# Kernel tuning notes

Measured on AMD Instinct MI355X. Metric: run time of the kernel, lower is better.

## Reference

```python
import jax, jax.numpy as jnp
import numpy as np

ALPHA = 0.5

def setup_inputs() -> dict:
    key = jax.random.key(0)
    k1, k2, k3 = jax.random.split(key, 3)
    B, C = 16384, 4096
    logits = jax.random.normal(k1, (B, C), dtype=jnp.float32)
    targets = jax.random.randint(k2, (B,), 0, C)
    hierarchy_matrix = jax.random.uniform(k3, (C, C), dtype=jnp.float32)
    return {"logits": logits, "targets": targets, "hierarchy_matrix": hierarchy_matrix}

def reference(logits, targets, hierarchy_matrix):
    # Cross-entropy (mean reduction)
    logp = jax.nn.log_softmax(logits, axis=-1)  # [B, C]
    ce = -jnp.take_along_axis(logp, targets[:, None], axis=-1).squeeze(-1).mean()
    # Hierarchical penalty: mean_i sum_c probs[i,c] * (1 + H[targets[i], c])
    probs = jnp.exp(logp)                        # [B, C]
    hier = hierarchy_matrix[targets]             # gather rows -> [B, C]
    penalty = (probs * (1.0 + hier)).sum(axis=-1).mean()
    return (1.0 - ALPHA) * ce + ALPHA * penalty
```

## Files before the change

### kernel.cpp

```cpp
#include <hip/hip_runtime.h>


#define ALPHA       0.5f
#define NCOLS       4096
#define WPB         4
#define BLOCK_THR   (WPB * 64)

__global__ __launch_bounds__(BLOCK_THR)
void hier_loss_partial(const float* __restrict__ logits,
                       const int*   __restrict__ targets,
                       const float* __restrict__ hmat,
                       float*       __restrict__ partials,
                       float inv_b)
{
    const int row  = blockIdx.x * WPB + (threadIdx.x >> 6);
    const int lane = threadIdx.x & 63;

    const float* __restrict__ lrow = logits + (size_t)row * NCOLS;
    const int    tgt               = targets[row];
    const float* __restrict__ hrow = hmat + (size_t)tgt * NCOLS;

    const float lt = lrow[tgt];

    const float4* __restrict__ l4 = reinterpret_cast<const float4*>(lrow);
    const float4* __restrict__ h4 = reinterpret_cast<const float4*>(hrow);

    float se = 0.0f;
    float sh = 0.0f;

    #pragma unroll
    for (int c = 0; c < 4; ++c) {
        float4 lv[4], hv[4];
        #pragma unroll
        for (int j = 0; j < 4; ++j) {
            lv[j] = l4[(c * 4 + j) * 64 + lane];
            hv[j] = h4[(c * 4 + j) * 64 + lane];
        }
        #pragma unroll
        for (int j = 0; j < 4; ++j) {
            const float e0 = __expf(lv[j].x);
            const float e1 = __expf(lv[j].y);
            const float e2 = __expf(lv[j].z);
            const float e3 = __expf(lv[j].w);
            se += (e0 + e1) + (e2 + e3);
            sh += e0 * hv[j].x + e1 * hv[j].y + e2 * hv[j].z + e3 * hv[j].w;
        }
    }

    #pragma unroll
    for (int off = 1; off < 64; off <<= 1) {
        se += __shfl_xor(se, off);
        sh += __shfl_xor(sh, off);
    }

    if (lane == 0) {
        const float ce  = __logf(se) - lt;
        const float pen = 1.0f + sh / se;
        partials[row] = ((1.0f - ALPHA) * ce + ALPHA * pen) * inv_b;
    }
}

__global__ __launch_bounds__(1024)
void hier_loss_reduce(const float* __restrict__ partials,
                      float*       __restrict__ out,
                      int n4)
{
    const int tid  = threadIdx.x;
    const int wave = tid >> 6;
    const int lane = tid & 63;

    const float4* __restrict__ p4 = reinterpret_cast<const float4*>(partials);
    float s = 0.0f;
    for (int i = tid; i < n4; i += 1024) {
        const float4 v = p4[i];
        s += (v.x + v.y) + (v.z + v.w);
    }

    #pragma unroll
    for (int off = 1; off < 64; off <<= 1)
        s += __shfl_xor(s, off);

    __shared__ float ss[16];
    if (lane == 0) ss[wave] = s;
    __syncthreads();

    if (tid == 0) {
        float acc = 0.0f;
        #pragma unroll
        for (int w = 0; w < 16; ++w) acc += ss[w];
        out[0] = acc;
    }
}

extern "C" void kernel_launch(void* const* d_in, const int* in_sizes, int n_in,
                              void* d_out, int out_size, void* d_ws, size_t ws_size,
                              hipStream_t stream)
{
    const float* logits  = (const float*)d_in[0];
    const int*   targets = (const int*)  d_in[1];
    const float* hmat    = (const float*)d_in[2];
    float*       out     = (float*)d_out;
    float*       ws      = (float*)d_ws;

    const int b = in_sizes[1];

    hier_loss_partial<<<b / WPB, BLOCK_THR, 0, stream>>>(logits, targets, hmat,
                                                         ws, 1.0f / (float)b);
    hier_loss_reduce<<<1, 1024, 0, stream>>>(ws, out, b / 4);
}
```

Before: 83.50 us.

## Bucket rows by target class to share each hierarchy row via LDS

```diff
diff --git a/kernel.cpp b/kernel.cpp
--- a/kernel.cpp
+++ b/kernel.cpp
@@ -1,62 +1,130 @@
 #include <hip/hip_runtime.h>
 
 
-#define ALPHA       0.5f
-#define NCOLS       4096
-#define WPB         4
-#define BLOCK_THR   (WPB * 64)
+#define ALPHA   0.5f
+#define NCOLS   4096
+#define NCLS    4096
 
-__global__ __launch_bounds__(BLOCK_THR)
-void hier_loss_partial(const float* __restrict__ logits,
-                       const int*   __restrict__ targets,
-                       const float* __restrict__ hmat,
-                       float*       __restrict__ partials,
-                       float inv_b)
+__global__ __launch_bounds__(1024)
+void bucket_rows(const int* __restrict__ targets, int n,
+                 int* __restrict__ gcnt, int* __restrict__ goff,
+                 int* __restrict__ order)
 {
-    const int row  = blockIdx.x * WPB + (threadIdx.x >> 6);
-    const int lane = threadIdx.x & 63;
+    __shared__ int h_cnt[NCLS];
+    __shared__ int h_cur[NCLS];
+    __shared__ int wtot[16];
 
-    const float* __restrict__ lrow = logits + (size_t)row * NCOLS;
-    const int    tgt               = targets[row];
-    const float* __restrict__ hrow = hmat + (size_t)tgt * NCOLS;
+    const int tid  = threadIdx.x;
+    const int wave = tid >> 6;
+    const int lane = tid & 63;
 
-    const float lt = lrow[tgt];
+    for (int i = tid; i < NCLS; i += 1024) h_cnt[i] = 0;
+    __syncthreads();
 
-    const float4* __restrict__ l4 = reinterpret_cast<const float4*>(lrow);
-    const float4* __restrict__ h4 = reinterpret_cast<const float4*>(hrow);
+    for (int i = tid; i < n; i += 1024)
+        atomicAdd(&h_cnt[targets[i]], 1);
+    __syncthreads();
 
-    float se = 0.0f;
-    float sh = 0.0f;
-
-    #pragma unroll
-    for (int c = 0; c < 4; ++c) {
-        float4 lv[4], hv[4];
-        #pragma unroll
-        for (int j = 0; j < 4; ++j) {
-            lv[j] = l4[(c * 4 + j) * 64 + lane];
-            hv[j] = h4[(c * 4 + j) * 64 + lane];
-        }
-        #pragma unroll
-        for (int j = 0; j < 4; ++j) {
-            const float e0 = __expf(lv[j].x);
-            const float e1 = __expf(lv[j].y);
-            const float e2 = __expf(lv[j].z);
-            const float e3 = __expf(lv[j].w);
-            se += (e0 + e1) + (e2 + e3);
-            sh += e0 * hv[j].x + e1 * hv[j].y + e2 * hv[j].z + e3 * hv[j].w;
-        }
-    }
-
+    const int base = tid * 4;
+    const int a0 = h_cnt[base+0], a1 = h_cnt[base+1];
+    const int a2 = h_cnt[base+2], a3 = h_cnt[base+3];
+    const int lsum = a0 + a1 + a2 + a3;
+    int incl = lsum;
     #pragma unroll
     for (int off = 1; off < 64; off <<= 1) {
-        se += __shfl_xor(se, off);
-        sh += __shfl_xor(sh, off);
+        int v = __shfl_up(incl, off);
+        if (lane >= off) incl += v;
     }
+    if (lane == 63) wtot[wave] = incl;
+    __syncthreads();
+    if (tid == 0) {
+        int run = 0;
+        for (int w = 0; w < 16; ++w) { int t = wtot[w]; wtot[w] = run; run += t; }
+    }
+    __syncthreads();
 
-    if (lane == 0) {
-        const float ce  = __logf(se) - lt;
-        const float pen = 1.0f + sh / se;
-        partials[row] = ((1.0f - ALPHA) * ce + ALPHA * pen) * inv_b;
+    const int off0 = wtot[wave] + (incl - lsum);
+    goff[base+0] = off0;
+    goff[base+1] = off0 + a0;
+    goff[base+2] = off0 + a0 + a1;
+    goff[base+3] = off0 + a0 + a1 + a2;
+    gcnt[base+0] = a0; gcnt[base+1] = a1; gcnt[base+2] = a2; gcnt[base+3] = a3;
+    h_cur[base+0] = off0;
+    h_cur[base+1] = off0 + a0;
+    h_cur[base+2] = off0 + a0 + a1;
+    h_cur[base+3] = off0 + a0 + a1 + a2;
+    __syncthreads();
+
+    for (int i = tid; i < n; i += 1024) {
+        const int pos = atomicAdd(&h_cur[targets[i]], 1);
+        order[pos] = i;
+    }
+}
+
+__global__ __launch_bounds__(256)
+void hier_main(const float* __restrict__ logits,
+               const float* __restrict__ hmat,
+               const int*   __restrict__ gcnt,
+               const int*   __restrict__ goff,
+               const int*   __restrict__ order,
+               float*       __restrict__ partials,
+               float inv_b)
+{
+    const int c     = blockIdx.x;
+    const int count = gcnt[c];
+    if (count == 0) return;
+    const int start = goff[c];
+    const int tid   = threadIdx.x;
+
+    __shared__ float hs[NCOLS];
+    {
+        const float4* h4 = reinterpret_cast<const float4*>(hmat + (size_t)c * NCOLS);
+        float4* s4 = reinterpret_cast<float4*>(hs);
+        #pragma unroll
+        for (int k = 0; k < 4; ++k)
+            s4[tid + k * 256] = h4[tid + k * 256];
+    }
+    __syncthreads();
+
+    const int wave = tid >> 6;
+    const int lane = tid & 63;
+    const float4* hs4 = reinterpret_cast<const float4*>(hs);
+
+    for (int r = wave; r < count; r += 4) {
+        const int row = order[start + r];
+        const float* __restrict__ lrow = logits + (size_t)row * NCOLS;
+        const float4* __restrict__ l4  = reinterpret_cast<const float4*>(lrow);
+        const float lt = lrow[c];
+
+        float se = 0.0f, sh = 0.0f;
+        #pragma unroll
+        for (int half = 0; half < 2; ++half) {
+            float4 lv[8];
+            #pragma unroll
+            for (int j = 0; j < 8; ++j)
+                lv[j] = l4[(half * 8 + j) * 64 + lane];
+            #pragma unroll
+            for (int j = 0; j < 8; ++j) {
+                const float4 hv = hs4[(half * 8 + j) * 64 + lane];
+                const float e0 = __expf(lv[j].x);
+                const float e1 = __expf(lv[j].y);
+                const float e2 = __expf(lv[j].z);
+                const float e3 = __expf(lv[j].w);
+                se += (e0 + e1) + (e2 + e3);
+                sh += e0 * hv.x + e1 * hv.y + e2 * hv.z + e3 * hv.w;
+            }
+        }
+
+        #pragma unroll
+        for (int off = 1; off < 64; off <<= 1) {
+            se += __shfl_xor(se, off);
+            sh += __shfl_xor(sh, off);
+        }
+        if (lane == 0) {
+            const float ce  = __logf(se) - lt;
+            const float pen = 1.0f + sh / se;
+            partials[row] = ((1.0f - ALPHA) * ce + ALPHA * pen) * inv_b;
+        }
     }
 }
 
@@ -75,7 +143,6 @@
         const float4 v = p4[i];
         s += (v.x + v.y) + (v.z + v.w);
     }
-
     #pragma unroll
     for (int off = 1; off < 64; off <<= 1)
         s += __shfl_xor(s, off);
@@ -83,7 +150,6 @@
     __shared__ float ss[16];
     if (lane == 0) ss[wave] = s;
     __syncthreads();
-
     if (tid == 0) {
         float acc = 0.0f;
         #pragma unroll
@@ -100,11 +166,16 @@
     const int*   targets = (const int*)  d_in[1];
     const float* hmat    = (const float*)d_in[2];
     float*       out     = (float*)d_out;
-    float*       ws      = (float*)d_ws;
 
     const int b = in_sizes[1];
 
-    hier_loss_partial<<<b / WPB, BLOCK_THR, 0, stream>>>(logits, targets, hmat,
-                                                         ws, 1.0f / (float)b);
-    hier_loss_reduce<<<1, 1024, 0, stream>>>(ws, out, b / 4);
+    int*   gcnt     = (int*)d_ws;
+    int*   goff     = gcnt + NCLS;
+    int*   order    = goff + NCLS;
+    float* partials = (float*)(order + b);
+
+    bucket_rows<<<1, 1024, 0, stream>>>(targets, b, gcnt, goff, order);
+    hier_main<<<NCLS, 256, 0, stream>>>(logits, hmat, gcnt, goff, order,
+                                        partials, 1.0f / (float)b);
+    hier_loss_reduce<<<1, 1024, 0, stream>>>(partials, out, b / 4);
 }
```

Result: no change. 84.53 us (+1.2%).
